# Optimization experiments

Hardware: AMD Instinct MI355X
Metric: run time of the kernel (lower is better)

Reference implementation:

```python
import jax, jax.numpy as jnp
import numpy as np

N_NODES = 20000
N_EDGES = 160000
D_IN = 512
D_OUT = 64


def _propagate(x, src, dst, num_nodes):
    # SLPropagate with add_self_loops=False, normalize=False:
    # out[dst] += x[src]  (plain sum aggregation over incoming edges)
    return jax.ops.segment_sum(x[src], dst, num_segments=num_nodes)


def setup_inputs() -> dict:
    key = jax.random.key(0)
    k1, k2, k3, k4 = jax.random.split(key, 4)
    x = jax.random.normal(k1, (N_NODES, D_IN), dtype=jnp.float32)
    edge_index = jax.random.randint(k2, (2, N_EDGES), 0, N_NODES, dtype=jnp.int64)
    # torch.nn.Linear default init scale ~ 1/sqrt(fan_in)
    s = 1.0 / np.sqrt(D_IN)
    W1 = jax.random.uniform(k3, (D_IN, D_IN), dtype=jnp.float32, minval=-s, maxval=s)
    W2 = jax.random.uniform(k4, (D_OUT, D_IN), dtype=jnp.float32, minval=-s, maxval=s)
    return {"x": x, "edge_index": edge_index, "W1": W1, "W2": W2}


def reference(x, edge_index, W1, W2):
    num_nodes = x.shape[0]
    src, dst = edge_index[0], edge_index[1]
    h = _propagate(x, src, dst, num_nodes)          # [N, D_IN]
    h = jax.nn.relu(jnp.einsum('nd,ed->ne', h, W1))  # lin1 (no bias) + relu
    h = _propagate(h, src, dst, num_nodes)          # [N, D_IN]
    h = jnp.einsum('nd,od->no', h, W2)              # lin2 (no bias) -> [N, D_OUT]
    return jax.nn.log_softmax(h, axis=1)
```

## Files before the change

kernel.cpp:

```cpp
#include <hip/hip_runtime.h>

#define D 512
#define DOUT 64
#define MAXDEG 64

typedef __bf16 bf16x8 __attribute__((ext_vector_type(8)));
typedef float floatx4 __attribute__((ext_vector_type(4)));

__device__ __forceinline__ void async_cp16(const void* g, void* lds) {
    __builtin_amdgcn_global_load_lds(
        (__attribute__((address_space(1))) void*)(void*)g,
        (__attribute__((address_space(3))) void*)lds, 16, 0, 0);
}

__global__ __launch_bounds__(256) void prep_kernel(
        int* __restrict__ cnt, int nN, int zeroBlocks,
        const float* __restrict__ x, __bf16* __restrict__ xb, int xN8,
        const float* __restrict__ W1, __bf16* __restrict__ w1b, int w1N8,
        const float* __restrict__ W2, __bf16* __restrict__ w2b, int w2N8) {
    int b = blockIdx.x;
    if (b < zeroBlocks) {
        int i4 = b * 1024 + threadIdx.x * 4;
        if (i4 + 3 < nN) *(int4*)(cnt + i4) = make_int4(0, 0, 0, 0);
        else {
            if (i4 + 0 < nN) cnt[i4 + 0] = 0;
            if (i4 + 1 < nN) cnt[i4 + 1] = 0;
            if (i4 + 2 < nN) cnt[i4 + 2] = 0;
        }
        return;
    }
    b -= zeroBlocks;
    int xBlocks = (xN8 + 255) >> 8;
    int w1Blocks = (w1N8 + 255) >> 8;
    const float* in; __bf16* outp; int n8;
    if (b < xBlocks) { in = x; outp = xb; n8 = xN8; }
    else if (b < xBlocks + w1Blocks) { b -= xBlocks; in = W1; outp = w1b; n8 = w1N8; }
    else { b -= xBlocks + w1Blocks; in = W2; outp = w2b; n8 = w2N8; }
    int i = b * 256 + threadIdx.x;
    if (i < n8) {
        const float4* p = (const float4*)in + (size_t)i * 2;
        float4 v0 = p[0], v1 = p[1];
        bf16x8 o;
        o[0] = (__bf16)v0.x; o[1] = (__bf16)v0.y; o[2] = (__bf16)v0.z; o[3] = (__bf16)v0.w;
        o[4] = (__bf16)v1.x; o[5] = (__bf16)v1.y; o[6] = (__bf16)v1.z; o[7] = (__bf16)v1.w;
        *((bf16x8*)outp + i) = o;
    }
}

__global__ __launch_bounds__(256) void gemm1_fill(
        const __bf16* __restrict__ A, const __bf16* __restrict__ B,
        __bf16* __restrict__ Cout, int M, int gemmBlocks,
        const int* __restrict__ src, const int* __restrict__ dst,
        int* __restrict__ cnt, int* __restrict__ col, int nE) {
    if (blockIdx.x >= gemmBlocks) {
        int base = (blockIdx.x - gemmBlocks) * 256 + threadIdx.x;
        int stride = (gridDim.x - gemmBlocks) * 256;
        for (int e = base; e < nE; e += stride) {
            int d = dst[e];
            int slot = atomicAdd(&cnt[d], 1);
            if (slot < MAXDEG) col[(size_t)d * MAXDEG + slot] = src[e];
        }
        return;
    }
    constexpr int BM = 128, BN = 128, BK = 64;
    __shared__ __bf16 As[8 * BM * 8];
    __shared__ __bf16 Bs[8 * BN * 8];

    const int tid = threadIdx.x;
    const int w = tid >> 6, lane = tid & 63;
    const int wrow = w >> 1, wcol = w & 1;
    const int m0 = (blockIdx.x >> 2) * BM, n0 = (blockIdx.x & 3) * BN;
    const int quad = lane >> 4, l15 = lane & 15;

    floatx4 acc[4][4] = {};

    for (int k0 = 0; k0 < D; k0 += BK) {
        #pragma unroll
        for (int c = 0; c < 4; ++c) {
            int ca = w * 4 + c;
            int kq = ca >> 1, sub = ca & 1;
            int row = m0 + sub * 64 + lane;
            if (row > M - 1) row = M - 1;
            async_cp16(A + (size_t)row * D + k0 + kq * 8, &As[(size_t)ca * 512]);
        }
        #pragma unroll
        for (int c = 0; c < 4; ++c) {
            int cb = w * 4 + c;
            int kq = cb >> 1, sub = cb & 1;
            int nn = n0 + sub * 64 + lane;
            async_cp16(B + (size_t)nn * D + k0 + kq * 8, &Bs[(size_t)cb * 512]);
        }
        __syncthreads();

        #pragma unroll
        for (int ksub = 0; ksub < 2; ++ksub) {
            bf16x8 af[4], bfr[4];
            #pragma unroll
            for (int mi = 0; mi < 4; ++mi)
                af[mi] = *(const bf16x8*)&As[(size_t)((ksub * 4 + quad) * BM
                                                      + wrow * 64 + mi * 16 + l15) * 8];
            #pragma unroll
            for (int nj = 0; nj < 4; ++nj)
                bfr[nj] = *(const bf16x8*)&Bs[(size_t)((ksub * 4 + quad) * BN
                                                       + wcol * 64 + nj * 16 + l15) * 8];
            #pragma unroll
            for (int mi = 0; mi < 4; ++mi)
                #pragma unroll
                for (int nj = 0; nj < 4; ++nj)
                    acc[mi][nj] = __builtin_amdgcn_mfma_f32_16x16x32_bf16(
                        af[mi], bfr[nj], acc[mi][nj], 0, 0, 0);
        }
        __syncthreads();
    }

    #pragma unroll
    for (int mi = 0; mi < 4; ++mi) {
        #pragma unroll
        for (int r = 0; r < 4; ++r) {
            int m = m0 + wrow * 64 + mi * 16 + quad * 4 + r;
            if (m < M) {
                #pragma unroll
                for (int nj = 0; nj < 4; ++nj) {
                    int n = n0 + wcol * 64 + nj * 16 + l15;
                    Cout[(size_t)m * D + n] = (__bf16)acc[mi][nj][r];
                }
            }
        }
    }
}

__global__ __launch_bounds__(256) void prop1_gemm2(
        const __bf16* __restrict__ t, const int* __restrict__ cnt,
        const int* __restrict__ col, const __bf16* __restrict__ B,
        __bf16* __restrict__ u, int nN) {
    __shared__ __bf16 As[16 * 512];
    __shared__ __bf16 Bs[4 * 64 * 8];

    const int tid = threadIdx.x;
    const int w = tid >> 6, lane = tid & 63;
    const int quad = lane >> 4, l15 = lane & 15;
    const int m0 = blockIdx.x * 16;

    for (int r = w; r < 16; r += 4) {
        int n = m0 + r;
        float acc0[8] = {}, acc1[8] = {};
        if (n < nN) {
            int deg = cnt[n]; if (deg > MAXDEG) deg = MAXDEG;
            const int* cp = col + (size_t)n * MAXDEG;
            int e = 0;
            for (; e + 8 <= deg; e += 8) {
                int s0 = cp[e],     s1_ = cp[e + 1], s2 = cp[e + 2], s3 = cp[e + 3];
                int s4 = cp[e + 4], s5 = cp[e + 5],  s6 = cp[e + 6], s7 = cp[e + 7];
                bf16x8 v0 = *(const bf16x8*)(t + (size_t)s0 * D + lane * 8);
                bf16x8 v1 = *(const bf16x8*)(t + (size_t)s1_ * D + lane * 8);
                bf16x8 v2 = *(const bf16x8*)(t + (size_t)s2 * D + lane * 8);
                bf16x8 v3 = *(const bf16x8*)(t + (size_t)s3 * D + lane * 8);
                bf16x8 v4 = *(const bf16x8*)(t + (size_t)s4 * D + lane * 8);
                bf16x8 v5 = *(const bf16x8*)(t + (size_t)s5 * D + lane * 8);
                bf16x8 v6 = *(const bf16x8*)(t + (size_t)s6 * D + lane * 8);
                bf16x8 v7 = *(const bf16x8*)(t + (size_t)s7 * D + lane * 8);
                #pragma unroll
                for (int i = 0; i < 8; ++i) {
                    acc0[i] += ((float)v0[i] + (float)v2[i]) + ((float)v4[i] + (float)v6[i]);
                    acc1[i] += ((float)v1[i] + (float)v3[i]) + ((float)v5[i] + (float)v7[i]);
                }
            }
            for (; e + 4 <= deg; e += 4) {
                int s0 = cp[e], s1_ = cp[e + 1], s2 = cp[e + 2], s3 = cp[e + 3];
                bf16x8 v0 = *(const bf16x8*)(t + (size_t)s0 * D + lane * 8);
                bf16x8 v1 = *(const bf16x8*)(t + (size_t)s1_ * D + lane * 8);
                bf16x8 v2 = *(const bf16x8*)(t + (size_t)s2 * D + lane * 8);
                bf16x8 v3 = *(const bf16x8*)(t + (size_t)s3 * D + lane * 8);
                #pragma unroll
                for (int i = 0; i < 8; ++i) {
                    acc0[i] += (float)v0[i] + (float)v2[i];
                    acc1[i] += (float)v1[i] + (float)v3[i];
                }
            }
            for (; e < deg; ++e) {
                int s0 = cp[e];
                bf16x8 v0 = *(const bf16x8*)(t + (size_t)s0 * D + lane * 8);
                #pragma unroll
                for (int i = 0; i < 8; ++i) acc0[i] += (float)v0[i];
            }
        }
        bf16x8 o;
        #pragma unroll
        for (int i = 0; i < 8; ++i) o[i] = (__bf16)fmaxf(acc0[i] + acc1[i], 0.f);
        int P = r * 64 + ((lane + r) & 63);
        *(bf16x8*)&As[(size_t)P * 8] = o;
    }
    __syncthreads();

    floatx4 acc = {};
    for (int k0 = 0; k0 < D; k0 += 32) {
        async_cp16(B + (size_t)lane * D + k0 + w * 8, &Bs[(size_t)w * 512]);
        __syncthreads();
        int g = (k0 >> 3) + quad;
        bf16x8 af = *(const bf16x8*)&As[(size_t)(l15 * 64 + ((g + l15) & 63)) * 8];
        bf16x8 bfr = *(const bf16x8*)&Bs[(size_t)(quad * 64 + w * 16 + l15) * 8];
        acc = __builtin_amdgcn_mfma_f32_16x16x32_bf16(af, bfr, acc, 0, 0, 0);
        __syncthreads();
    }

    #pragma unroll
    for (int r = 0; r < 4; ++r) {
        int m = m0 + quad * 4 + r;
        if (m < nN)
            u[(size_t)m * DOUT + w * 16 + l15] = (__bf16)acc[r];
    }
}

__global__ __launch_bounds__(256) void prop2_lsm(const __bf16* __restrict__ u,
        const int* __restrict__ cnt, const int* __restrict__ col,
        float* __restrict__ out, int nN) {
    int n = blockIdx.x * 4 + (threadIdx.x >> 6);
    if (n >= nN) return;
    int lane = threadIdx.x & 63;
    int deg = cnt[n]; if (deg > MAXDEG) deg = MAXDEG;
    const int* cp = col + (size_t)n * MAXDEG;
    float a0 = 0.f, a1 = 0.f, a2 = 0.f, a3 = 0.f;
    float a4 = 0.f, a5 = 0.f, a6 = 0.f, a7 = 0.f;
    int e = 0;
    for (; e + 8 <= deg; e += 8) {
        int s0 = cp[e],     s1 = cp[e + 1], s2 = cp[e + 2], s3 = cp[e + 3];
        int s4 = cp[e + 4], s5 = cp[e + 5], s6 = cp[e + 6], s7 = cp[e + 7];
        a0 += (float)u[(size_t)s0 * DOUT + lane];
        a1 += (float)u[(size_t)s1 * DOUT + lane];
        a2 += (float)u[(size_t)s2 * DOUT + lane];
        a3 += (float)u[(size_t)s3 * DOUT + lane];
        a4 += (float)u[(size_t)s4 * DOUT + lane];
        a5 += (float)u[(size_t)s5 * DOUT + lane];
        a6 += (float)u[(size_t)s6 * DOUT + lane];
        a7 += (float)u[(size_t)s7 * DOUT + lane];
    }
    for (; e + 4 <= deg; e += 4) {
        int s0 = cp[e], s1 = cp[e + 1], s2 = cp[e + 2], s3 = cp[e + 3];
        a0 += (float)u[(size_t)s0 * DOUT + lane];
        a1 += (float)u[(size_t)s1 * DOUT + lane];
        a2 += (float)u[(size_t)s2 * DOUT + lane];
        a3 += (float)u[(size_t)s3 * DOUT + lane];
    }
    for (; e < deg; ++e) a0 += (float)u[(size_t)cp[e] * DOUT + lane];
    float v = ((a0 + a4) + (a1 + a5)) + ((a2 + a6) + (a3 + a7));
    float mx = v;
    #pragma unroll
    for (int off = 32; off >= 1; off >>= 1) mx = fmaxf(mx, __shfl_xor(mx, off, 64));
    float s = expf(v - mx);
    #pragma unroll
    for (int off = 32; off >= 1; off >>= 1) s += __shfl_xor(s, off, 64);
    out[(size_t)n * DOUT + lane] = v - mx - logf(s);
}


extern "C" void kernel_launch(void* const* d_in, const int* in_sizes, int n_in,
                              void* d_out, int out_size, void* d_ws, size_t ws_size,
                              hipStream_t stream) {
    const float* x  = (const float*)d_in[0];
    const int*   ei = (const int*)d_in[1];
    const float* W1 = (const float*)d_in[2];
    const float* W2 = (const float*)d_in[3];
    float* out = (float*)d_out;

    const int N = in_sizes[0] / D;
    const int E = in_sizes[1] / 2;
    const int* src = ei;
    const int* dst = ei + E;

    size_t off = 0;
    auto alloc = [&](size_t bytes) -> void* {
        void* p = (char*)d_ws + off;
        off = (off + bytes + 255) & ~(size_t)255;
        return p;
    };
    int*    cnt     = (int*)alloc(sizeof(int) * (size_t)N);
    int*    col     = (int*)alloc(sizeof(int) * (size_t)N * MAXDEG);
    __bf16* w1b     = (__bf16*)alloc(sizeof(__bf16) * (size_t)D * D);
    __bf16* w2b     = (__bf16*)alloc(sizeof(__bf16) * (size_t)DOUT * D);
    __bf16* xb      = (__bf16*)alloc(sizeof(__bf16) * (size_t)N * D);
    __bf16* t       = (__bf16*)alloc(sizeof(__bf16) * (size_t)N * D);
    __bf16* u       = (__bf16*)alloc(sizeof(__bf16) * (size_t)N * DOUT);

    const int zeroBlocks = (N + 1023) / 1024;
    const int xN8 = N * D / 8, w1N8 = D * D / 8, w2N8 = DOUT * D / 8;
    const int cvtBlocks = (xN8 + 255) / 256 + (w1N8 + 255) / 256 + (w2N8 + 255) / 256;

    prep_kernel<<<zeroBlocks + cvtBlocks, 256, 0, stream>>>(
        cnt, N, zeroBlocks, x, xb, xN8, W1, w1b, w1N8, W2, w2b, w2N8);

    const int gemmBlocks = ((N + 127) / 128) * 4;
    gemm1_fill<<<gemmBlocks + 64, 256, 0, stream>>>(
        xb, w1b, t, N, gemmBlocks, src, dst, cnt, col, E);

    prop1_gemm2<<<(N + 15) / 16, 256, 0, stream>>>(t, cnt, col, w2b, u, N);

    prop2_lsm<<<(N + 3) / 4, 256, 0, stream>>>(u, cnt, col, out, N);
}
```

Before: 169.6 us.

## Interleave four rows' gathers per wave with a zero sentinel row, keep W2 in registers

In the fused prop1+gemm2 kernel, each wave now gathers its four rows at the same time, in batches of four neighbours. Indices are read as int4, and padded slots point at a zeroed sentinel row appended to t, so the loop has no tail branches and keeps up to sixteen independent row loads in flight. The W2 fragments are preloaded into registers before the MFMA loop, which removes the per-k LDS staging and the two barriers per iteration. The cost is higher register pressure, plus wasted loads on the sentinel when row degrees in a block are unequal.

```diff
diff --git a/kernel.cpp b/kernel.cpp
--- a/kernel.cpp
+++ b/kernel.cpp
@@ -15,6 +15,7 @@
 
 __global__ __launch_bounds__(256) void prep_kernel(
         int* __restrict__ cnt, int nN, int zeroBlocks,
+        __bf16* __restrict__ tzero,
         const float* __restrict__ x, __bf16* __restrict__ xb, int xN8,
         const float* __restrict__ W1, __bf16* __restrict__ w1b, int w1N8,
         const float* __restrict__ W2, __bf16* __restrict__ w2b, int w2N8) {
@@ -30,6 +31,11 @@
         return;
     }
     b -= zeroBlocks;
+    if (b == 0) {
+        ((unsigned*)tzero)[threadIdx.x] = 0u;
+        return;
+    }
+    b -= 1;
     int xBlocks = (xN8 + 255) >> 8;
     int w1Blocks = (w1N8 + 255) >> 8;
     const float* in; __bf16* outp; int n8;
@@ -134,80 +140,82 @@
         const int* __restrict__ col, const __bf16* __restrict__ B,
         __bf16* __restrict__ u, int nN) {
     __shared__ __bf16 As[16 * 512];
-    __shared__ __bf16 Bs[4 * 64 * 8];
 
     const int tid = threadIdx.x;
     const int w = tid >> 6, lane = tid & 63;
     const int quad = lane >> 4, l15 = lane & 15;
     const int m0 = blockIdx.x * 16;
 
-    for (int r = w; r < 16; r += 4) {
-        int n = m0 + r;
-        float acc0[8] = {}, acc1[8] = {};
-        if (n < nN) {
-            int deg = cnt[n]; if (deg > MAXDEG) deg = MAXDEG;
-            const int* cp = col + (size_t)n * MAXDEG;
-            int e = 0;
-            for (; e + 8 <= deg; e += 8) {
-                int s0 = cp[e],     s1_ = cp[e + 1], s2 = cp[e + 2], s3 = cp[e + 3];
-                int s4 = cp[e + 4], s5 = cp[e + 5],  s6 = cp[e + 6], s7 = cp[e + 7];
-                bf16x8 v0 = *(const bf16x8*)(t + (size_t)s0 * D + lane * 8);
-                bf16x8 v1 = *(const bf16x8*)(t + (size_t)s1_ * D + lane * 8);
-                bf16x8 v2 = *(const bf16x8*)(t + (size_t)s2 * D + lane * 8);
-                bf16x8 v3 = *(const bf16x8*)(t + (size_t)s3 * D + lane * 8);
-                bf16x8 v4 = *(const bf16x8*)(t + (size_t)s4 * D + lane * 8);
-                bf16x8 v5 = *(const bf16x8*)(t + (size_t)s5 * D + lane * 8);
-                bf16x8 v6 = *(const bf16x8*)(t + (size_t)s6 * D + lane * 8);
-                bf16x8 v7 = *(const bf16x8*)(t + (size_t)s7 * D + lane * 8);
-                #pragma unroll
-                for (int i = 0; i < 8; ++i) {
-                    acc0[i] += ((float)v0[i] + (float)v2[i]) + ((float)v4[i] + (float)v6[i]);
-                    acc1[i] += ((float)v1[i] + (float)v3[i]) + ((float)v5[i] + (float)v7[i]);
-                }
-            }
-            for (; e + 4 <= deg; e += 4) {
-                int s0 = cp[e], s1_ = cp[e + 1], s2 = cp[e + 2], s3 = cp[e + 3];
-                bf16x8 v0 = *(const bf16x8*)(t + (size_t)s0 * D + lane * 8);
-                bf16x8 v1 = *(const bf16x8*)(t + (size_t)s1_ * D + lane * 8);
-                bf16x8 v2 = *(const bf16x8*)(t + (size_t)s2 * D + lane * 8);
-                bf16x8 v3 = *(const bf16x8*)(t + (size_t)s3 * D + lane * 8);
-                #pragma unroll
-                for (int i = 0; i < 8; ++i) {
-                    acc0[i] += (float)v0[i] + (float)v2[i];
-                    acc1[i] += (float)v1[i] + (float)v3[i];
-                }
-            }
-            for (; e < deg; ++e) {
-                int s0 = cp[e];
-                bf16x8 v0 = *(const bf16x8*)(t + (size_t)s0 * D + lane * 8);
-                #pragma unroll
-                for (int i = 0; i < 8; ++i) acc0[i] += (float)v0[i];
-            }
-        }
+    int deg[4];
+    const int4* ip[4];
+    float acc[4][8] = {};
+    int maxb = 0;
+    #pragma unroll
+    for (int q = 0; q < 4; ++q) {
+        int n = m0 + w + q * 4;
+        int nc = (n < nN) ? n : 0;
+        int d = 0;
+        if (n < nN) { d = cnt[n]; if (d > MAXDEG) d = MAXDEG; }
+        deg[q] = d;
+        ip[q] = (const int4*)(col + (size_t)nc * MAXDEG);
+        int bq = (d + 3) >> 2;
+        if (bq > maxb) maxb = bq;
+    }
+
+    for (int b = 0; b < maxb; ++b) {
+        int s[4][4];
+        #pragma unroll
+        for (int q = 0; q < 4; ++q) {
+            int4 i4 = ip[q][b];
+            int e0 = b * 4;
+            s[q][0] = (e0 + 0 < deg[q]) ? i4.x : nN;
+            s[q][1] = (e0 + 1 < deg[q]) ? i4.y : nN;
+            s[q][2] = (e0 + 2 < deg[q]) ? i4.z : nN;
+            s[q][3] = (e0 + 3 < deg[q]) ? i4.w : nN;
+        }
+        bf16x8 v[4][4];
+        #pragma unroll
+        for (int q = 0; q < 4; ++q)
+            #pragma unroll
+            for (int j = 0; j < 4; ++j)
+                v[q][j] = *(const bf16x8*)(t + (size_t)s[q][j] * D + lane * 8);
+        #pragma unroll
+        for (int q = 0; q < 4; ++q)
+            #pragma unroll
+            for (int i = 0; i < 8; ++i)
+                acc[q][i] += ((float)v[q][0][i] + (float)v[q][1][i])
+                           + ((float)v[q][2][i] + (float)v[q][3][i]);
+    }
+
+    bf16x8 breg[16];
+    #pragma unroll
+    for (int kq = 0; kq < 16; ++kq)
+        breg[kq] = *(const bf16x8*)(B + (size_t)(w * 16 + l15) * D + kq * 32 + quad * 8);
+
+    #pragma unroll
+    for (int q = 0; q < 4; ++q) {
+        int r = w + q * 4;
         bf16x8 o;
         #pragma unroll
-        for (int i = 0; i < 8; ++i) o[i] = (__bf16)fmaxf(acc0[i] + acc1[i], 0.f);
+        for (int i = 0; i < 8; ++i) o[i] = (__bf16)fmaxf(acc[q][i], 0.f);
         int P = r * 64 + ((lane + r) & 63);
         *(bf16x8*)&As[(size_t)P * 8] = o;
     }
     __syncthreads();
 
-    floatx4 acc = {};
-    for (int k0 = 0; k0 < D; k0 += 32) {
-        async_cp16(B + (size_t)lane * D + k0 + w * 8, &Bs[(size_t)w * 512]);
-        __syncthreads();
-        int g = (k0 >> 3) + quad;
+    floatx4 c = {};
+    #pragma unroll
+    for (int kq = 0; kq < 16; ++kq) {
+        int g = kq * 4 + quad;
         bf16x8 af = *(const bf16x8*)&As[(size_t)(l15 * 64 + ((g + l15) & 63)) * 8];
-        bf16x8 bfr = *(const bf16x8*)&Bs[(size_t)(quad * 64 + w * 16 + l15) * 8];
-        acc = __builtin_amdgcn_mfma_f32_16x16x32_bf16(af, bfr, acc, 0, 0, 0);
-        __syncthreads();
+        c = __builtin_amdgcn_mfma_f32_16x16x32_bf16(af, breg[kq], c, 0, 0, 0);
     }
 
     #pragma unroll
     for (int r = 0; r < 4; ++r) {
         int m = m0 + quad * 4 + r;
         if (m < nN)
-            u[(size_t)m * DOUT + w * 16 + l15] = (__bf16)acc[r];
+            u[(size_t)m * DOUT + w * 16 + l15] = (__bf16)c[r];
     }
 }
 
@@ -278,15 +286,15 @@
     __bf16* w1b     = (__bf16*)alloc(sizeof(__bf16) * (size_t)D * D);
     __bf16* w2b     = (__bf16*)alloc(sizeof(__bf16) * (size_t)DOUT * D);
     __bf16* xb      = (__bf16*)alloc(sizeof(__bf16) * (size_t)N * D);
-    __bf16* t       = (__bf16*)alloc(sizeof(__bf16) * (size_t)N * D);
+    __bf16* t       = (__bf16*)alloc(sizeof(__bf16) * (size_t)(N + 1) * D);
     __bf16* u       = (__bf16*)alloc(sizeof(__bf16) * (size_t)N * DOUT);
 
     const int zeroBlocks = (N + 1023) / 1024;
     const int xN8 = N * D / 8, w1N8 = D * D / 8, w2N8 = DOUT * D / 8;
     const int cvtBlocks = (xN8 + 255) / 256 + (w1N8 + 255) / 256 + (w2N8 + 255) / 256;
 
-    prep_kernel<<<zeroBlocks + cvtBlocks, 256, 0, stream>>>(
-        cnt, N, zeroBlocks, x, xb, xN8, W1, w1b, w1N8, W2, w2b, w2N8);
+    prep_kernel<<<zeroBlocks + 1 + cvtBlocks, 256, 0, stream>>>(
+        cnt, N, zeroBlocks, t + (size_t)N * D, x, xb, xN8, W1, w1b, w1N8, W2, w2b, w2N8);
 
     const int gemmBlocks = ((N + 127) / 128) * 4;
     gemm1_fill<<<gemmBlocks + 64, 256, 0, stream>>>(
```

New measurement: 168.7 us. Within noise of the previous version (-0.5%).
